# Performance work log

Hardware: AMD Instinct MI355X
Metric: run time of the kernel (lower is better)

## Reference

```python
import jax, jax.numpy as jnp
import numpy as np

N = 30000      # nodes
K = 32         # in-degree per node (before self loop)
NFEAT = 512
NHID = 128
NCLASS = 64


def setup_inputs() -> dict:
    key = jax.random.key(0)
    k1, k2, k3, k4 = jax.random.split(key, 4)
    x = jax.random.normal(k1, (N, NFEAT), dtype=jnp.float32)
    # neighbor offsets in [0, N-2]; src = (dst + off + 1) % N guarantees src != dst
    neighbors = jax.random.randint(k2, (N, K), 0, N - 1)
    W1 = jax.random.normal(k3, (NFEAT, NHID), dtype=jnp.float32) / np.float32(np.sqrt(NFEAT))
    b1 = jnp.zeros((NHID,), dtype=jnp.float32)
    W2 = jax.random.normal(k4, (NHID, NCLASS), dtype=jnp.float32) / np.float32(np.sqrt(NHID))
    b2 = jnp.zeros((NCLASS,), dtype=jnp.float32)
    return {"x": x, "neighbors": neighbors, "W1": W1, "b1": b1, "W2": W2, "b2": b2}


def _median_conv(x, nbrs_all, W, b):
    # x: [N, Fin]; nbrs_all: [N, D] neighbor indices (self loop included)
    h = x @ W                          # [N, Fout]
    gathered = h[nbrs_all]             # [N, D, Fout]
    d = nbrs_all.shape[1]
    # torch .median(dim=1) returns the lower median: sorted index (d-1)//2
    med = jnp.sort(gathered, axis=1)[:, (d - 1) // 2]  # [N, Fout]
    return med + b


def reference(x, neighbors, W1, b1, W2, b2):
    n = x.shape[0]
    dst = jnp.arange(n)
    src = (dst[:, None] + neighbors + 1) % n            # no self loops (remove_self_loops)
    nbrs_all = jnp.concatenate([src, dst[:, None]], axis=1)  # add_self_loops -> degree K+1
    # dropout is identity at eval time
    h = jax.nn.relu(_median_conv(x, nbrs_all, W1, b1))
    out = _median_conv(h, nbrs_all, W2, b2)
    return jax.nn.log_softmax(out, axis=1)
```

## Files before the change

kernel.cpp:

```cpp
#include <hip/hip_runtime.h>
#include <math.h>

static constexpr int NN = 30000;
static constexpr int NF = 512;
static constexpr int NH = 128;
static constexpr int NC = 64;

__device__ __forceinline__ void cswap(float& a, float& b) {
  float lo = fminf(a, b), hi = fmaxf(a, b);
  a = lo; b = hi;
}

__device__ __forceinline__ void sort32(float v[32]) {
  #pragma unroll
  for (int k = 2; k <= 32; k <<= 1) {
    #pragma unroll
    for (int j = k >> 1; j > 0; j >>= 1) {
      #pragma unroll
      for (int i = 0; i < 32; ++i) {
        const int l = i ^ j;
        if (l > i) {
          if ((i & k) == 0) cswap(v[i], v[l]);
          else              cswap(v[l], v[i]);
        }
      }
    }
  }
}

__global__ __launch_bounds__(256) void k1_gemm1(const float* __restrict__ x,
                                                const float* __restrict__ W1,
                                                float* __restrict__ h0) {
  __shared__ float As[32][68];
  __shared__ float Bs[32][128];
  const int tid = threadIdx.x;
  const int m0  = blockIdx.x * 64;
  const int tc  = tid & 15;
  const int tr  = tid >> 4;

  float acc[4][8];
  #pragma unroll
  for (int r = 0; r < 4; ++r)
    #pragma unroll
    for (int c = 0; c < 8; ++c) acc[r][c] = 0.f;

  for (int k0 = 0; k0 < NF; k0 += 32) {
    #pragma unroll
    for (int it = 0; it < 2; ++it) {
      const int p   = tid + it * 256;
      const int row = p >> 3;
      const int c4  = p & 7;
      int grow = m0 + row;
      if (grow > NN - 1) grow = NN - 1;
      const float4 a = *reinterpret_cast<const float4*>(&x[grow * NF + k0 + c4 * 4]);
      As[c4 * 4 + 0][row] = a.x;
      As[c4 * 4 + 1][row] = a.y;
      As[c4 * 4 + 2][row] = a.z;
      As[c4 * 4 + 3][row] = a.w;
    }
    #pragma unroll
    for (int it = 0; it < 4; ++it) {
      const int p   = tid + it * 256;
      const int row = p >> 5;
      const int c4  = p & 31;
      *reinterpret_cast<float4*>(&Bs[row][c4 * 4]) =
          *reinterpret_cast<const float4*>(&W1[(k0 + row) * NH + c4 * 4]);
    }
    __syncthreads();

    #pragma unroll
    for (int kk = 0; kk < 32; ++kk) {
      const float4 a  = *reinterpret_cast<const float4*>(&As[kk][tr * 4]);
      const float4 b0 = *reinterpret_cast<const float4*>(&Bs[kk][tc * 8]);
      const float4 b1 = *reinterpret_cast<const float4*>(&Bs[kk][tc * 8 + 4]);
      const float av[4] = {a.x, a.y, a.z, a.w};
      const float bv[8] = {b0.x, b0.y, b0.z, b0.w, b1.x, b1.y, b1.z, b1.w};
      #pragma unroll
      for (int r = 0; r < 4; ++r)
        #pragma unroll
        for (int c = 0; c < 8; ++c)
          acc[r][c] = fmaf(av[r], bv[c], acc[r][c]);
    }
    __syncthreads();
  }

  #pragma unroll
  for (int r = 0; r < 4; ++r) {
    const int grow = m0 + tr * 4 + r;
    if (grow < NN) {
      const float4 o0 = make_float4(acc[r][0], acc[r][1], acc[r][2], acc[r][3]);
      const float4 o1 = make_float4(acc[r][4], acc[r][5], acc[r][6], acc[r][7]);
      *reinterpret_cast<float4*>(&h0[grow * NH + tc * 8 + 0]) = o0;
      *reinterpret_cast<float4*>(&h0[grow * NH + tc * 8 + 4]) = o1;
    }
  }
}

__global__ __launch_bounds__(256) void k2_median1_gemm2(const float* __restrict__ h0,
                                                        const int* __restrict__ nbr,
                                                        const float* __restrict__ b1,
                                                        const float* __restrict__ W2,
                                                        float* __restrict__ z) {
  __shared__ int   nb[2][32];
  __shared__ float hs[2][NH];
  const int tid = threadIdx.x;
  const int g   = tid >> 7;
  const int f   = tid & 127;
  const int i   = blockIdx.x * 2 + g;

  if (f < 32) nb[g][f] = nbr[i * 32 + f];
  __syncthreads();

  float v[32];
  #pragma unroll
  for (int k = 0; k < 32; ++k) {
    int idx = i + nb[g][k] + 1;
    if (idx >= NN) idx -= NN;
    v[k] = h0[idx * NH + f];
  }
  const float self = h0[i * NH + f];

  sort32(v);
  const float med = fminf(fmaxf(self, v[15]), v[16]);
  const float h   = fmaxf(med + b1[f], 0.f);

  hs[g][f] = h;
  __syncthreads();

  if (f < NC) {
    float acc = 0.f;
    #pragma unroll 8
    for (int kk = 0; kk < NH; ++kk)
      acc = fmaf(hs[g][kk], W2[kk * NC + f], acc);
    z[i * NC + f] = acc;
  }
}

__global__ __launch_bounds__(256) void k3_median2_lsm(const float* __restrict__ z,
                                                      const int* __restrict__ nbr,
                                                      const float* __restrict__ b2,
                                                      float* __restrict__ out) {
  __shared__ int nb[4][32];
  const int tid = threadIdx.x;
  const int g   = tid >> 6;
  const int f   = tid & 63;
  const int i   = blockIdx.x * 4 + g;

  if (f < 32) nb[g][f] = nbr[i * 32 + f];
  __syncthreads();

  float v[32];
  #pragma unroll
  for (int k = 0; k < 32; ++k) {
    int idx = i + nb[g][k] + 1;
    if (idx >= NN) idx -= NN;
    v[k] = z[idx * NC + f];
  }
  const float self = z[i * NC + f];

  sort32(v);
  const float med = fminf(fmaxf(self, v[15]), v[16]);
  const float o   = med + b2[f];

  float m = o;
  #pragma unroll
  for (int d = 1; d < 64; d <<= 1) m = fmaxf(m, __shfl_xor(m, d, 64));
  float e = __expf(o - m);
  float s = e;
  #pragma unroll
  for (int d = 1; d < 64; d <<= 1) s += __shfl_xor(s, d, 64);

  out[i * NC + f] = (o - m) - __logf(s);
}

extern "C" void kernel_launch(void* const* d_in, const int* in_sizes, int n_in,
                              void* d_out, int out_size, void* d_ws, size_t ws_size,
                              hipStream_t stream) {
  const float* x   = (const float*)d_in[0];
  const int*   nbr = (const int*)d_in[1];
  const float* W1  = (const float*)d_in[2];
  const float* b1  = (const float*)d_in[3];
  const float* W2  = (const float*)d_in[4];
  const float* b2  = (const float*)d_in[5];
  float* outp = (float*)d_out;

  float* h0 = (float*)d_ws;
  float* zz = (float*)((char*)d_ws + (size_t)NN * NH * 4);

  k1_gemm1<<<(NN + 63) / 64, 256, 0, stream>>>(x, W1, h0);
  k2_median1_gemm2<<<NN / 2, 256, 0, stream>>>(h0, nbr, b1, W2, zz);
  k3_median2_lsm<<<NN / 4, 256, 0, stream>>>(zz, nbr, b2, outp);
}
```

Before: 257.5 us.

## Store intermediates in bf16, pack two features per lane, cheaper median selection

Intermediate h0 and z are now stored as bf16 and each lane gathers a packed pair of features, which halves gather traffic and doubles per-thread work in the median kernels. The full 32-element bitonic sort is replaced by two sorted 16-element halves plus a merge-based selection of ranks 15/16. GEMM1 tiles grow to 128 rows with an 8x8 register accumulator. The bf16 rounding of intermediates can change medians and lose accuracy relative to the fp32 reference.

```diff
diff --git a/kernel.cpp b/kernel.cpp
--- a/kernel.cpp
+++ b/kernel.cpp
@@ -1,4 +1,5 @@
 #include <hip/hip_runtime.h>
+#include <hip/hip_bf16.h>
 #include <math.h>
 
 static constexpr int NN = 30000;
@@ -6,53 +7,69 @@
 static constexpr int NH = 128;
 static constexpr int NC = 64;
 
+typedef unsigned int uint32;
+
+__device__ __forceinline__ float bf_lo(uint32 p) { return __uint_as_float(p << 16); }
+__device__ __forceinline__ float bf_hi(uint32 p) { return __uint_as_float(p & 0xffff0000u); }
+
 __device__ __forceinline__ void cswap(float& a, float& b) {
   float lo = fminf(a, b), hi = fmaxf(a, b);
   a = lo; b = hi;
 }
 
-__device__ __forceinline__ void sort32(float v[32]) {
-  #pragma unroll
-  for (int k = 2; k <= 32; k <<= 1) {
+__device__ __forceinline__ void medsel32(float v[32], float& m15, float& m16) {
+  #pragma unroll
+  for (int k = 2; k <= 16; k <<= 1) {
     #pragma unroll
     for (int j = k >> 1; j > 0; j >>= 1) {
       #pragma unroll
-      for (int i = 0; i < 32; ++i) {
-        const int l = i ^ j;
-        if (l > i) {
-          if ((i & k) == 0) cswap(v[i], v[l]);
-          else              cswap(v[l], v[i]);
+      for (int h = 0; h < 2; ++h) {
+        #pragma unroll
+        for (int i = 0; i < 16; ++i) {
+          const int l = i ^ j;
+          if (l > i) {
+            const int a = h * 16 + i, b = h * 16 + l;
+            if ((i & k) == 0) cswap(v[a], v[b]);
+            else              cswap(v[b], v[a]);
+          }
         }
       }
     }
   }
+  m15 = fminf(v[0], v[31]);
+  m16 = fmaxf(v[0], v[31]);
+  #pragma unroll
+  for (int i = 1; i < 16; ++i) {
+    m15 = fmaxf(m15, fminf(v[i], v[31 - i]));
+    m16 = fminf(m16, fmaxf(v[i], v[31 - i]));
+  }
 }
 
 __global__ __launch_bounds__(256) void k1_gemm1(const float* __restrict__ x,
                                                 const float* __restrict__ W1,
-                                                float* __restrict__ h0) {
-  __shared__ float As[32][68];
+                                                __hip_bfloat16* __restrict__ h0b) {
+  __shared__ float As[32][132];
   __shared__ float Bs[32][128];
   const int tid = threadIdx.x;
-  const int m0  = blockIdx.x * 64;
+  const int m0  = blockIdx.x * 128;
+  const int tr  = tid >> 4;
   const int tc  = tid & 15;
-  const int tr  = tid >> 4;
-
-  float acc[4][8];
-  #pragma unroll
-  for (int r = 0; r < 4; ++r)
+
+  float acc[8][8];
+  #pragma unroll
+  for (int r = 0; r < 8; ++r)
     #pragma unroll
     for (int c = 0; c < 8; ++c) acc[r][c] = 0.f;
 
   for (int k0 = 0; k0 < NF; k0 += 32) {
     #pragma unroll
-    for (int it = 0; it < 2; ++it) {
+    for (int it = 0; it < 4; ++it) {
       const int p   = tid + it * 256;
       const int row = p >> 3;
       const int c4  = p & 7;
-      int grow = m0 + row;
-      if (grow > NN - 1) grow = NN - 1;
-      const float4 a = *reinterpret_cast<const float4*>(&x[grow * NF + k0 + c4 * 4]);
+      int gr = m0 + row;
+      if (gr >= NN) gr = NN - 1;
+      const float4 a = *reinterpret_cast<const float4*>(&x[(size_t)gr * NF + k0 + c4 * 4]);
       As[c4 * 4 + 0][row] = a.x;
       As[c4 * 4 + 1][row] = a.y;
       As[c4 * 4 + 2][row] = a.z;
@@ -70,13 +87,14 @@
 
     #pragma unroll
     for (int kk = 0; kk < 32; ++kk) {
-      const float4 a  = *reinterpret_cast<const float4*>(&As[kk][tr * 4]);
-      const float4 b0 = *reinterpret_cast<const float4*>(&Bs[kk][tc * 8]);
+      const float4 a0 = *reinterpret_cast<const float4*>(&As[kk][tr * 8 + 0]);
+      const float4 a1 = *reinterpret_cast<const float4*>(&As[kk][tr * 8 + 4]);
+      const float4 b0 = *reinterpret_cast<const float4*>(&Bs[kk][tc * 8 + 0]);
       const float4 b1 = *reinterpret_cast<const float4*>(&Bs[kk][tc * 8 + 4]);
-      const float av[4] = {a.x, a.y, a.z, a.w};
+      const float av[8] = {a0.x, a0.y, a0.z, a0.w, a1.x, a1.y, a1.z, a1.w};
       const float bv[8] = {b0.x, b0.y, b0.z, b0.w, b1.x, b1.y, b1.z, b1.w};
       #pragma unroll
-      for (int r = 0; r < 4; ++r)
+      for (int r = 0; r < 8; ++r)
         #pragma unroll
         for (int c = 0; c < 8; ++c)
           acc[r][c] = fmaf(av[r], bv[c], acc[r][c]);
@@ -85,92 +103,109 @@
   }
 
   #pragma unroll
-  for (int r = 0; r < 4; ++r) {
-    const int grow = m0 + tr * 4 + r;
-    if (grow < NN) {
-      const float4 o0 = make_float4(acc[r][0], acc[r][1], acc[r][2], acc[r][3]);
-      const float4 o1 = make_float4(acc[r][4], acc[r][5], acc[r][6], acc[r][7]);
-      *reinterpret_cast<float4*>(&h0[grow * NH + tc * 8 + 0]) = o0;
-      *reinterpret_cast<float4*>(&h0[grow * NH + tc * 8 + 4]) = o1;
-    }
-  }
-}
-
-__global__ __launch_bounds__(256) void k2_median1_gemm2(const float* __restrict__ h0,
+  for (int r = 0; r < 8; ++r) {
+    const int gr = m0 + tr * 8 + r;
+    if (gr < NN) {
+      alignas(16) __hip_bfloat16 t[8];
+      #pragma unroll
+      for (int c = 0; c < 8; ++c) t[c] = __float2bfloat16(acc[r][c]);
+      *reinterpret_cast<uint4*>(&h0b[(size_t)gr * NH + tc * 8]) =
+          *reinterpret_cast<const uint4*>(t);
+    }
+  }
+}
+
+__global__ __launch_bounds__(256) void k2_median1_gemm2(const __hip_bfloat16* __restrict__ h0b,
                                                         const int* __restrict__ nbr,
                                                         const float* __restrict__ b1,
                                                         const float* __restrict__ W2,
-                                                        float* __restrict__ z) {
-  __shared__ int   nb[2][32];
-  __shared__ float hs[2][NH];
-  const int tid = threadIdx.x;
-  const int g   = tid >> 7;
-  const int f   = tid & 127;
-  const int i   = blockIdx.x * 2 + g;
-
-  if (f < 32) nb[g][f] = nbr[i * 32 + f];
+                                                        __hip_bfloat16* __restrict__ zb) {
+  __shared__ int   nb[4][32];
+  __shared__ float hs[4][NH];
+  const int tid  = threadIdx.x;
+  const int g    = tid >> 6;
+  const int lane = tid & 63;
+  const int i    = blockIdx.x * 4 + g;
+
+  if (lane < 32) nb[g][lane] = nbr[i * 32 + lane];
   __syncthreads();
 
-  float v[32];
+  const uint32* hrow = reinterpret_cast<const uint32*>(h0b);
+  uint32 pr[32];
   #pragma unroll
   for (int k = 0; k < 32; ++k) {
     int idx = i + nb[g][k] + 1;
     if (idx >= NN) idx -= NN;
-    v[k] = h0[idx * NH + f];
-  }
-  const float self = h0[i * NH + f];
-
-  sort32(v);
-  const float med = fminf(fmaxf(self, v[15]), v[16]);
-  const float h   = fmaxf(med + b1[f], 0.f);
-
-  hs[g][f] = h;
+    pr[k] = hrow[idx * 64 + lane];
+  }
+  const uint32 ps = hrow[i * 64 + lane];
+
+  float v[32], m15, m16;
+  #pragma unroll
+  for (int k = 0; k < 32; ++k) v[k] = bf_lo(pr[k]);
+  medsel32(v, m15, m16);
+  const float hA = fmaxf(fminf(fmaxf(bf_lo(ps), m15), m16) + b1[lane * 2 + 0], 0.f);
+
+  #pragma unroll
+  for (int k = 0; k < 32; ++k) v[k] = bf_hi(pr[k]);
+  medsel32(v, m15, m16);
+  const float hB = fmaxf(fminf(fmaxf(bf_hi(ps), m15), m16) + b1[lane * 2 + 1], 0.f);
+
+  hs[g][lane * 2 + 0] = hA;
+  hs[g][lane * 2 + 1] = hB;
   __syncthreads();
 
-  if (f < NC) {
-    float acc = 0.f;
-    #pragma unroll 8
-    for (int kk = 0; kk < NH; ++kk)
-      acc = fmaf(hs[g][kk], W2[kk * NC + f], acc);
-    z[i * NC + f] = acc;
-  }
-}
-
-__global__ __launch_bounds__(256) void k3_median2_lsm(const float* __restrict__ z,
+  float acc = 0.f;
+  #pragma unroll 16
+  for (int kk = 0; kk < NH; ++kk)
+    acc = fmaf(hs[g][kk], W2[kk * NC + lane], acc);
+  zb[i * NC + lane] = __float2bfloat16(acc);
+}
+
+__global__ __launch_bounds__(256) void k3_median2_lsm(const __hip_bfloat16* __restrict__ zb,
                                                       const int* __restrict__ nbr,
                                                       const float* __restrict__ b2,
                                                       float* __restrict__ out) {
-  __shared__ int nb[4][32];
-  const int tid = threadIdx.x;
-  const int g   = tid >> 6;
-  const int f   = tid & 63;
-  const int i   = blockIdx.x * 4 + g;
-
-  if (f < 32) nb[g][f] = nbr[i * 32 + f];
+  __shared__ int nb[8][32];
+  const int tid  = threadIdx.x;
+  const int g    = tid >> 5;
+  const int lane = tid & 31;
+  const int i    = blockIdx.x * 8 + g;
+
+  nb[g][lane] = nbr[i * 32 + lane];
   __syncthreads();
 
-  float v[32];
+  const uint32* zrow = reinterpret_cast<const uint32*>(zb);
+  uint32 pr[32];
   #pragma unroll
   for (int k = 0; k < 32; ++k) {
     int idx = i + nb[g][k] + 1;
     if (idx >= NN) idx -= NN;
-    v[k] = z[idx * NC + f];
-  }
-  const float self = z[i * NC + f];
-
-  sort32(v);
-  const float med = fminf(fmaxf(self, v[15]), v[16]);
-  const float o   = med + b2[f];
-
-  float m = o;
-  #pragma unroll
-  for (int d = 1; d < 64; d <<= 1) m = fmaxf(m, __shfl_xor(m, d, 64));
-  float e = __expf(o - m);
-  float s = e;
-  #pragma unroll
-  for (int d = 1; d < 64; d <<= 1) s += __shfl_xor(s, d, 64);
-
-  out[i * NC + f] = (o - m) - __logf(s);
+    pr[k] = zrow[idx * 32 + lane];
+  }
+  const uint32 ps = zrow[i * 32 + lane];
+
+  float v[32], m15, m16;
+  #pragma unroll
+  for (int k = 0; k < 32; ++k) v[k] = bf_lo(pr[k]);
+  medsel32(v, m15, m16);
+  const float oA = fminf(fmaxf(bf_lo(ps), m15), m16) + b2[lane * 2 + 0];
+
+  #pragma unroll
+  for (int k = 0; k < 32; ++k) v[k] = bf_hi(pr[k]);
+  medsel32(v, m15, m16);
+  const float oB = fminf(fmaxf(bf_hi(ps), m15), m16) + b2[lane * 2 + 1];
+
+  float m = fmaxf(oA, oB);
+  #pragma unroll
+  for (int d = 1; d < 32; d <<= 1) m = fmaxf(m, __shfl_xor(m, d, 32));
+  float s = __expf(oA - m) + __expf(oB - m);
+  #pragma unroll
+  for (int d = 1; d < 32; d <<= 1) s += __shfl_xor(s, d, 32);
+  const float ls = __logf(s);
+
+  *reinterpret_cast<float2*>(&out[i * NC + lane * 2]) =
+      make_float2(oA - m - ls, oB - m - ls);
 }
 
 extern "C" void kernel_launch(void* const* d_in, const int* in_sizes, int n_in,
@@ -184,10 +219,10 @@
   const float* b2  = (const float*)d_in[5];
   float* outp = (float*)d_out;
 
-  float* h0 = (float*)d_ws;
-  float* zz = (float*)((char*)d_ws + (size_t)NN * NH * 4);
-
-  k1_gemm1<<<(NN + 63) / 64, 256, 0, stream>>>(x, W1, h0);
-  k2_median1_gemm2<<<NN / 2, 256, 0, stream>>>(h0, nbr, b1, W2, zz);
-  k3_median2_lsm<<<NN / 4, 256, 0, stream>>>(zz, nbr, b2, outp);
-}
+  __hip_bfloat16* h0b = (__hip_bfloat16*)d_ws;
+  __hip_bfloat16* zb  = (__hip_bfloat16*)((char*)d_ws + (size_t)NN * NH * 2);
+
+  k1_gemm1<<<(NN + 127) / 128, 256, 0, stream>>>(x, W1, h0b);
+  k2_median1_gemm2<<<NN / 4, 256, 0, stream>>>(h0b, nbr, b1, W2, zb);
+  k3_median2_lsm<<<NN / 8, 256, 0, stream>>>(zb, nbr, b2, outp);
+}
```

After: 254.8 us. About the same (-1.1%).
